# Kernel tuning notes

Measured on AMD Instinct MI355X. Metric: run time of the kernel, lower is better.

The kernel has to match this reference:

```python
import jax, jax.numpy as jnp
import numpy as np

B, N, L, C, H = 2, 3000, 6, 128, 1
IN_DIM = 6
SIGMA_D = 1.0
EPS = 1e-5
DH = C // H


def _conv1(x, W, b):
    # pointwise Conv1d: x [B,Cin,N], W [Cout,Cin], b [Cout]
    return jnp.einsum('oc,bcn->bon', W, x) + b[None, :, None]


def _bn(x, g, beta):
    # BatchNorm1d (training-mode batch stats) over (B, N) per channel
    m = x.mean(axis=(0, 2), keepdims=True)
    v = x.var(axis=(0, 2), keepdims=True)
    return g[None, :, None] * (x - m) * jax.lax.rsqrt(v + EPS) + beta[None, :, None]


def setup_inputs() -> dict:
    key = jax.random.key(0)
    ks = iter(jax.random.split(key, 80))

    def w(shape, fan_in):
        return jax.random.normal(next(ks), shape, jnp.float32) * (1.0 / np.sqrt(fan_in))

    src = jax.random.normal(next(ks), (B, N, 3), jnp.float32)
    tgt = src + 0.1 * jax.random.normal(next(ks), (B, N, 3), jnp.float32)
    corr_pos = jnp.concatenate([src, tgt], axis=-1)  # [B,N,6]

    d = {
        'corr_pos': corr_pos, 'src_keypts': src, 'tgt_keypts': tgt,
        'init_W': w((C, IN_DIM), IN_DIM), 'init_b': jnp.zeros((C,), jnp.float32),
        'pcn_W': w((L, C, C), C), 'pcn_b': jnp.zeros((L, C), jnp.float32),
        'pcn_g': jnp.ones((L, C), jnp.float32), 'pcn_beta': jnp.zeros((L, C), jnp.float32),
        'qW': w((L, C, C), C), 'qb': jnp.zeros((L, C), jnp.float32),
        'kW': w((L, C, C), C), 'kb': jnp.zeros((L, C), jnp.float32),
        'vW': w((L, C, C), C), 'vb': jnp.zeros((L, C), jnp.float32),
        'm1W': w((L, C // 2, C), C), 'm1b': jnp.zeros((L, C // 2), jnp.float32),
        'm1g': jnp.ones((L, C // 2), jnp.float32), 'm1beta': jnp.zeros((L, C // 2), jnp.float32),
        'm2W': w((L, C // 2, C // 2), C // 2), 'm2b': jnp.zeros((L, C // 2), jnp.float32),
        'm2g': jnp.ones((L, C // 2), jnp.float32), 'm2beta': jnp.zeros((L, C // 2), jnp.float32),
        'm3W': w((L, C, C // 2), C // 2), 'm3b': jnp.zeros((L, C), jnp.float32),
        'c1W': w((32, C), C), 'c1b': jnp.zeros((32,), jnp.float32),
        'c2W': w((32, 32), 32), 'c2b': jnp.zeros((32,), jnp.float32),
        'c3W': w((1, 32), 32), 'c3b': jnp.zeros((1,), jnp.float32),
    }
    return d


def reference(corr_pos, src_keypts, tgt_keypts, init_W, init_b,
              pcn_W, pcn_b, pcn_g, pcn_beta,
              qW, qb, kW, kb, vW, vb,
              m1W, m1b, m1g, m1beta, m2W, m2b, m2g, m2beta, m3W, m3b,
              c1W, c1b, c2W, c2b, c3W, c3b):
    # spatial compatibility: clamp(1 - (d_src - d_tgt)^2 / sigma_d^2, min=0)  [B,N,N]
    src_dist = jnp.linalg.norm(src_keypts[:, :, None, :] - src_keypts[:, None, :, :], axis=-1)
    tgt_dist = jnp.linalg.norm(tgt_keypts[:, :, None, :] - tgt_keypts[:, None, :, :], axis=-1)
    sc = jnp.maximum(1.0 - (src_dist - tgt_dist) ** 2 / SIGMA_D ** 2, 0.0)

    # init embedding: [B,C,N]
    x = _conv1(jnp.swapaxes(corr_pos, 1, 2), init_W, init_b)
    scale = 1.0 / jnp.sqrt(jnp.float32(DH))

    for i in range(L):
        # PointCN layer
        x = jax.nn.relu(_bn(_conv1(x, pcn_W[i], pcn_b[i]), pcn_g[i], pcn_beta[i]))
        # NonLocal block
        Q = _conv1(x, qW[i], qb[i]).reshape(B, H, DH, N)
        K = _conv1(x, kW[i], kb[i]).reshape(B, H, DH, N)
        V = _conv1(x, vW[i], vb[i]).reshape(B, H, DH, N)
        scores = jnp.einsum('bhco,bhci->bhoi', Q, K) * scale  # [B,H,N,N]
        weight = jax.nn.softmax(sc[:, None, :, :] * scores, axis=-1)
        msg = jnp.einsum('bhoi,bhci->bhco', weight, V).reshape(B, C, N)
        msg = jax.nn.relu(_bn(_conv1(msg, m1W[i], m1b[i]), m1g[i], m1beta[i]))
        msg = jax.nn.relu(_bn(_conv1(msg, m2W[i], m2b[i]), m2g[i], m2beta[i]))
        msg = _conv1(msg, m3W[i], m3b[i])
        x = x + msg

    corr_feat = x
    norm = jnp.maximum(jnp.linalg.norm(corr_feat, axis=1, keepdims=True), 1e-12)
    normed_corr_feat = corr_feat / norm
    h = jax.nn.relu(_conv1(corr_feat, c1W, c1b))
    h = jax.nn.relu(_conv1(h, c2W, c2b))
    confidence = _conv1(h, c3W, c3b)[:, 0, :]  # [B,N]
    return confidence, normed_corr_feat
```

## Files before the change

kernel.cpp:

```cpp
#include <hip/hip_runtime.h>
#include <hip/hip_bf16.h>


#define BB 2
#define NN 3000
#define CC 128
#define LAYERS 6
#define BN_EPS 1e-5f
#define ATT_SCALE 0.08838834764831845f
#define INV_CNT (1.f / (float)(BB * NN))

typedef _Float16 f16;
typedef _Float16 f16x8 __attribute__((ext_vector_type(8)));
typedef float f32x4 __attribute__((ext_vector_type(4)));

__global__ void init_conv(const float* __restrict__ corr, const float* __restrict__ W,
                          const float* __restrict__ bias, float* __restrict__ x) {
  int idx = blockIdx.x * 256 + threadIdx.x;
  if (idx >= BB * CC * NN) return;
  int n = idx % NN;
  int c = (idx / NN) % CC;
  int b = idx / (NN * CC);
  const float* cp = corr + (b * NN + n) * 6;
  float acc = bias[c];
#pragma unroll
  for (int d = 0; d < 6; ++d) acc += W[c * 6 + d] * cp[d];
  x[idx] = acc;
}

__launch_bounds__(256)
__global__ void conv_mfma_pcn(const float* __restrict__ Xg, float* __restrict__ Y,
                              const float* __restrict__ W, const float* __restrict__ bias,
                              float* __restrict__ osums) {
  __shared__ f16 Xsh[32][136], Xsl[32][136];
  __shared__ f16 Wsh[128][40], Wsl[128][40];
  const int tid = threadIdx.x;
// ... 194 lines not shown
      if (p < BB * NN) {
        int b = p / NN, n = p % NN;
#pragma unroll
        for (int r = 0; r < 4; ++r) {
          int co = co0 + ct * 16 + quad * 4 + r;
          float v = acc[ct][pt][r] + bias[co];
          f16 h = (f16)v;
          f16 lo = (f16)(v - (float)h);
          if (sel == 0) {
            size_t o = (size_t)(b * NN + n) * CC + co;
            Qh[o] = h; Ql[o] = lo;
          } else if (sel == 1) {
            size_t o = (size_t)(b * NN + n) * CC + co;
            Kh[o] = h; Kl[o] = lo;
          } else {
            size_t o = (size_t)(b * CC + co) * NN + n;
            Vh[o] = h; Vl[o] = lo;
          }
        }
      }
    }
}

template <int CIN, int COUT, int NP, int MODE, int CSPLIT, int BNIN, int STATS>
__launch_bounds__(256)
__global__ void conv_k(const float* __restrict__ in, float* __restrict__ out,
                       const float* __restrict__ W, const float* __restrict__ bias,
                       const float* __restrict__ res,
                       const float* __restrict__ isums, const float* __restrict__ ig,
                       const float* __restrict__ ibeta,
                       const float* __restrict__ rsums, const float* __restrict__ rg,
                       const float* __restrict__ rbeta, float* __restrict__ osums) {
  constexpr int COB = COUT / CSPLIT;
  constexpr int CH = (CIN > 64) ? 64 : CIN;
  constexpr int PG = NP / 4;
  constexpr int KPT = COB * PG / 256;
  constexpr int XROW = (NP == 16) ? 20 : 32;
  __shared__ alignas(16) float Xs[CIN][XROW];
  __shared__ float Ws[COB][CH + 1];
  __shared__ float bnsc[BNIN ? CIN : 1], bnsh[BNIN ? CIN : 1];
  const int tid = threadIdx.x;
  const int p0 = blockIdx.x * NP;
  const int co0 = blockIdx.y * COB;

  if (BNIN) {
    for (int c = tid; c < CIN; c += 256) {
      float s = isums[c], s2 = isums[CIN + c];
      float mean = s * INV_CNT;
      float var = s2 * INV_CNT - mean * mean;
      float sc = ig[c] * rsqrtf(var + BN_EPS);
      bnsc[c] = sc;
      bnsh[c] = ibeta[c] - mean * sc;
    }
    __syncthreads();
  }

  for (int idx = tid; idx < CIN * NP; idx += 256) {
    int ci = idx / NP, j = idx % NP;
    int p = p0 + j;
    float v = 0.f;
    if (p < BB * NN) {
      int b = p / NN, n = p % NN;
      v = in[(b * CIN + ci) * NN + n];
      if (BNIN) {
        v = v * bnsc[ci] + bnsh[ci];
        v = v > 0.f ? v : 0.f;
      }
    }
    Xs[ci][j] = v;
  }

  const int nb = (tid % PG) * 4;
  const int cb = (tid / PG) * KPT;

  float acc[KPT][4];
#pragma unroll
  for (int k = 0; k < KPT; ++k)
#pragma unroll
    for (int j = 0; j < 4; ++j) acc[k][j] = 0.f;

  for (int c0 = 0; c0 < CIN; c0 += CH) {
    __syncthreads();
    for (int idx = tid; idx < COB * CH; idx += 256) {
      int co = idx / CH, cc = idx % CH;
      Ws[co][cc] = W[(co0 + co) * CIN + c0 + cc];
    }
    __syncthreads();
#pragma unroll 4
    for (int cc = 0; cc < CH; ++cc) {
      float4 xv = *reinterpret_cast<const float4*>(&Xs[c0 + cc][nb]);
#pragma unroll
      for (int k = 0; k < KPT; ++k) {
        float w = Ws[cb + k][cc];
        acc[k][0] += w * xv.x;
        acc[k][1] += w * xv.y;
        acc[k][2] += w * xv.z;
        acc[k][3] += w * xv.w;
      }
    }
  }

#pragma unroll
  for (int k = 0; k < KPT; ++k) {
    int co = co0 + cb + k;
    float bv = bias[co];
    float rsc = 0.f, rsh = 0.f;
    if (MODE == 3) {
      float s = rsums[co], s2 = rsums[COUT + co];
      float mean = s * INV_CNT;
      float var = s2 * INV_CNT - mean * mean;
      rsc = rg[co] * rsqrtf(var + BN_EPS);
      rsh = rbeta[co] - mean * rsc;
    }
    float sp = 0.f, sp2 = 0.f;
#pragma unroll
    for (int j = 0; j < 4; ++j) {
      int p = p0 + nb + j;
      if (p < BB * NN) {
        int b = p / NN, n = p % NN;
        int o = (b * COUT + co) * NN + n;
        float v = acc[k][j] + bv;
        if (MODE == 3) {
          float rr = res[o] * rsc + rsh;
          v += (rr > 0.f ? rr : 0.f);
        }
        out[o] = v;
        if (STATS) {
          sp += v;
          sp2 += v * v;
        }
      }
    }
    if (STATS) {
#pragma unroll
      for (int d = 1; d < PG; d <<= 1) {
        sp += __shfl_xor(sp, d);
        sp2 += __shfl_xor(sp2, d);
      }
      if ((tid & (PG - 1)) == 0) {
        atomicAdd(&osums[co], sp);
        atomicAdd(&osums[COUT + co], sp2);
      }
    }
  }
}

__launch_bounds__(512)
__global__ void attn_mf7(const f16* __restrict__ Qhp, const f16* __restrict__ Qlp,
                         const f16* __restrict__ Khp, const f16* __restrict__ Klp,
                         const f16* __restrict__ Vhp, const f16* __restrict__ Vlp,
                         const float* __restrict__ srcp, const float* __restrict__ tgtp,
                         float* __restrict__ pacc, float* __restrict__ pm,
                         float* __restrict__ pl, int chunk) {
  const int b = blockIdx.z;
  const int q0 = blockIdx.x * 128;
  const int s = blockIdx.y;
  const int cs = s * chunk;
  const int ce = min(cs + chunk, NN);
  const int tid = threadIdx.x;
  const int w = tid >> 6, lane = tid & 63, quad = lane >> 4, l15 = lane & 15;

  __shared__ f16 Ksh[32][136], Ksl[32][136];
  __shared__ f16 Vsh[128][40], Vsl[128][40];
  __shared__ f16 Ps[8][16][40];
  __shared__ float kps[6][36];

  float qp[4][6];
  const int orow = q0 + w * 16;
#pragma unroll
  for (int r = 0; r < 4; ++r) {
    int o = orow + quad * 4 + r;
    if (o >= NN) o = NN - 1;
#pragma unroll
    for (int d = 0; d < 3; ++d) {
      qp[r][d] = srcp[(b * NN + o) * 3 + d];
      qp[r][3 + d] = tgtp[(b * NN + o) * 3 + d];
    }
  }
  f16x8 qh[4], ql[4];
  {
    int o = orow + l15;
    if (o >= NN) o = NN - 1;
    size_t base = (size_t)(b * NN + o) * CC + quad * 8;
#pragma unroll
    for (int cc = 0; cc < 4; ++cc) {
      qh[cc] = *reinterpret_cast<const f16x8*>(Qhp + base + cc * 32);
      ql[cc] = *reinterpret_cast<const f16x8*>(Qlp + base + cc * 32);
    }
  }

  float m[4], l[4];
#pragma unroll
  for (int r = 0; r < 4; ++r) {
    m[r] = -1e30f;
    l[r] = 0.f;
  }
  f32x4 acco[8];
#pragma unroll
  for (int t = 0; t < 8; ++t) acco[t] = (f32x4){0.f, 0.f, 0.f, 0.f};

  const int NT = (ce - cs + 31) >> 5;
  for (int it = 0; it < NT; ++it) {
    const int kk0 = cs + it * 32;
    __syncthreads();
    for (int t = tid; t < 1024; t += 512) {
      int plane = t >> 9, row = (t >> 4) & 31, cu = t & 15;
      int kr = kk0 + row;
      if (kr >= NN) kr = NN - 1;
      const f16* src = (plane ? Klp : Khp) + (size_t)(b * NN + kr) * CC + cu * 8;
      uint4 v = *reinterpret_cast<const uint4*>(src);
      f16* dst = plane ? &Ksl[row][cu * 8] : &Ksh[row][cu * 8];
      *reinterpret_cast<uint4*>(dst) = v;
    }
    for (int t = tid; t < 1024; t += 512) {
      int plane = t >> 9, c = (t >> 2) & 127, iu = t & 3;
      int kb = kk0 + iu * 8;
      if (kb > NN - 8) kb = NN - 8;
      const f16* src = (plane ? Vlp : Vhp) + (size_t)(b * CC + c) * NN + kb;
      uint4 v = *reinterpret_cast<const uint4*>(src);
      f16* dst = plane ? &Vsl[c][iu * 8] : &Vsh[c][iu * 8];
      *reinterpret_cast<uint4*>(dst) = v;
    }
    if (tid < 192) {
      int d = tid >> 5, i = tid & 31;
      int ig = kk0 + i;
      if (ig >= NN) ig = NN - 1;
      kps[d][i] = (d < 3) ? srcp[(b * NN + ig) * 3 + d] : tgtp[(b * NN + ig) * 3 + d - 3];
    }
    __syncthreads();

    f32x4 accs[2];
#pragma unroll
    for (int k4 = 0; k4 < 2; ++k4) accs[k4] = (f32x4){0.f, 0.f, 0.f, 0.f};
#pragma unroll
    for (int cc = 0; cc < 4; ++cc) {
#pragma unroll
      for (int k4 = 0; k4 < 2; ++k4) {
        f16x8 bh = *reinterpret_cast<const f16x8*>(&Ksh[k4 * 16 + l15][cc * 32 + quad * 8]);
        f16x8 bl = *reinterpret_cast<const f16x8*>(&Ksl[k4 * 16 + l15][cc * 32 + quad * 8]);
        accs[k4] = __builtin_amdgcn_mfma_f32_16x16x32_f16(qh[cc], bl, accs[k4], 0, 0, 0);
        accs[k4] = __builtin_amdgcn_mfma_f32_16x16x32_f16(ql[cc], bh, accs[k4], 0, 0, 0);
        accs[k4] = __builtin_amdgcn_mfma_f32_16x16x32_f16(qh[cc], bh, accs[k4], 0, 0, 0);
      }
    }

    float sv[2][4];
#pragma unroll
    for (int k4 = 0; k4 < 2; ++k4) {
      int iloc = k4 * 16 + l15;
      int ig = kk0 + iloc;
      float kx = kps[0][iloc], ky = kps[1][iloc], kz = kps[2][iloc];
      float tx = kps[3][iloc], ty = kps[4][iloc], tz = kps[5][iloc];
#pragma unroll
      for (int r = 0; r < 4; ++r) {
        float dx = qp[r][0] - kx, dy = qp[r][1] - ky, dz = qp[r][2] - kz;
        float ds2 = dx * dx + dy * dy + dz * dz;
        float ex = qp[r][3] - tx, ey = qp[r][4] - ty, ez = qp[r][5] - tz;
        float dt2 = ex * ex + ey * ey + ez * ez;
        float d2 = ds2 + dt2 - 2.f * sqrtf(ds2 * dt2);
        float gg = 1.f - d2;
        gg = gg > 0.f ? gg : 0.f;
        float val = accs[k4][r] * (ATT_SCALE * gg);
        sv[k4][r] = (ig < ce) ? val : -1e30f;
      }
    }

    float tmax[4];
#pragma unroll
    for (int r = 0; r < 4; ++r) tmax[r] = fmaxf(sv[0][r], sv[1][r]);
#pragma unroll
    for (int d = 1; d <= 8; d <<= 1)
#pragma unroll
      for (int r = 0; r < 4; ++r) tmax[r] = fmaxf(tmax[r], __shfl_xor(tmax[r], d));

    float alpha[4], ps[4];
    f16 pf[2][4];
#pragma unroll
    for (int r = 0; r < 4; ++r) {
      float mn = fmaxf(m[r], tmax[r]);
      alpha[r] = __expf(m[r] - mn);
      m[r] = mn;
      pf[0][r] = (f16)__expf(sv[0][r] - mn);
      pf[1][r] = (f16)__expf(sv[1][r] - mn);
      ps[r] = (float)pf[0][r] + (float)pf[1][r];
    }
#pragma unroll
    for (int d = 1; d <= 8; d <<= 1)
#pragma unroll
      for (int r = 0; r < 4; ++r) ps[r] += __shfl_xor(ps[r], d);
#pragma unroll
    for (int r = 0; r < 4; ++r) {
      l[r] = l[r] * alpha[r] + ps[r];
#pragma unroll
      for (int t = 0; t < 8; ++t) acco[t][r] *= alpha[r];
    }
#pragma unroll
    for (int r = 0; r < 4; ++r) {
      Ps[w][quad * 4 + r][l15] = pf[0][r];
      Ps[w][quad * 4 + r][16 + l15] = pf[1][r];
    }
    __syncthreads();

    {
      f16x8 af = *reinterpret_cast<const f16x8*>(&Ps[w][l15][quad * 8]);
#pragma unroll
      for (int t = 0; t < 8; ++t) {
        f16x8 vh = *reinterpret_cast<const f16x8*>(&Vsh[t * 16 + l15][quad * 8]);
        f16x8 vl = *reinterpret_cast<const f16x8*>(&Vsl[t * 16 + l15][quad * 8]);
        acco[t] = __builtin_amdgcn_mfma_f32_16x16x32_f16(af, vl, acco[t], 0, 0, 0);
        acco[t] = __builtin_amdgcn_mfma_f32_16x16x32_f16(af, vh, acco[t], 0, 0, 0);
      }
    }
  }

  const int pidx = s * BB + b;
  if (l15 == 0) {
#pragma unroll
    for (int r = 0; r < 4; ++r) {
      int o = orow + quad * 4 + r;
      if (o < NN) {
        pm[pidx * NN + o] = m[r];
        pl[pidx * NN + o] = l[r];
      }
    }
  }
#pragma unroll
  for (int r = 0; r < 4; ++r) {
    int o = orow + quad * 4 + r;
    if (o < NN) {
      size_t base2 = ((size_t)pidx * NN + o) * CC;
#pragma unroll
      for (int t = 0; t < 8; ++t) pacc[base2 + t * 16 + l15] = acco[t][r];
    }
  }
}

__launch_bounds__(256)
__global__ void conv_m1(const float* __restrict__ pacc, const float* __restrict__ pm,
                        const float* __restrict__ pl, float* __restrict__ out,
                        const float* __restrict__ W, const float* __restrict__ bias,
                        float* __restrict__ osums, int ksplit) {
  __shared__ alignas(16) float Xs[128][20];
  __shared__ float Ws[64][65];
  __shared__ float Es[16][17];
  __shared__ float Li[16];
  const int tid = threadIdx.x;
  const int p0 = blockIdx.x * 16;

  if (tid < 16) {
    int p = p0 + tid;
    float Lv = 1.f;
    if (p < BB * NN) {
      int b = p / NN, o = p % NN;
      float M = -1e30f;
      for (int s = 0; s < ksplit; ++s) M = fmaxf(M, pm[(s * BB + b) * NN + o]);
      Lv = 0.f;
      for (int s = 0; s < ksplit; ++s) {
        int pi = s * BB + b;
        float e = __expf(pm[pi * NN + o] - M);
        Es[tid][s] = e;
        Lv += pl[pi * NN + o] * e;
      }
    } else {
      for (int s = 0; s < ksplit; ++s) Es[tid][s] = 0.f;
    }
    Li[tid] = 1.f / Lv;
  }
  __syncthreads();

  for (int idx = tid; idx < 512; idx += 256) {
    int j = idx >> 5, c4 = (idx & 31) * 4;
    int p = p0 + j;
    float4 a = {0.f, 0.f, 0.f, 0.f};
    if (p < BB * NN) {
      int b = p / NN, o = p % NN;
      for (int s = 0; s < ksplit; ++s) {
        float e = Es[j][s];
        const float4 pv = *reinterpret_cast<const float4*>(
            &pacc[((size_t)(s * BB + b) * NN + o) * CC + c4]);
        a.x += pv.x * e;
        a.y += pv.y * e;
        a.z += pv.z * e;
        a.w += pv.w * e;
      }
      float inv = Li[j];
      a.x *= inv; a.y *= inv; a.z *= inv; a.w *= inv;
    }
    Xs[c4][j] = a.x;
    Xs[c4 + 1][j] = a.y;
    Xs[c4 + 2][j] = a.z;
    Xs[c4 + 3][j] = a.w;
  }

  const int nb = (tid & 3) * 4;
  const int co = tid >> 2;
  float acc[4] = {0.f, 0.f, 0.f, 0.f};

  for (int c0 = 0; c0 < 128; c0 += 64) {
    __syncthreads();
    for (int idx = tid; idx < 64 * 64; idx += 256) {
      int cr = idx >> 6, cc = idx & 63;
      Ws[cr][cc] = W[cr * 128 + c0 + cc];
    }
    __syncthreads();
#pragma unroll 4
    for (int cc = 0; cc < 64; ++cc) {
      float4 xv = *reinterpret_cast<const float4*>(&Xs[c0 + cc][nb]);
      float w = Ws[co][cc];
      acc[0] += w * xv.x;
      acc[1] += w * xv.y;
      acc[2] += w * xv.z;
      acc[3] += w * xv.w;
    }
  }

  {
    float bv = bias[co];
    float sp = 0.f, sp2 = 0.f;
#pragma unroll
    for (int j = 0; j < 4; ++j) {
      int p = p0 + nb + j;
      if (p < BB * NN) {
        int b = p / NN, n = p % NN;
        float v = acc[j] + bv;
        out[(b * 64 + co) * NN + n] = v;
        sp += v;
        sp2 += v * v;
      }
    }
    sp += __shfl_xor(sp, 1);
    sp2 += __shfl_xor(sp2, 1);
    sp += __shfl_xor(sp, 2);
    sp2 += __shfl_xor(sp2, 2);
    if ((tid & 3) == 0) {
      atomicAdd(&osums[co], sp);
      atomicAdd(&osums[64 + co], sp2);
    }
  }
}

__launch_bounds__(256)
__global__ void head_all(const float* __restrict__ Xg,
                         const float* __restrict__ c1W, const float* __restrict__ c1b,
                         const float* __restrict__ c2W, const float* __restrict__ c2b,
                         const float* __restrict__ c3W, const float* __restrict__ c3b,
                         float* __restrict__ out) {
  __shared__ float Xs[128][33];
  __shared__ float W1[32][129];
  __shared__ float W2[32][33];
  __shared__ float Hs[32][33], H2s[32][33];
  __shared__ float Inv[32];
  const int tid = threadIdx.x;
  const int p0 = blockIdx.x * 32;
  const int j = tid >> 3, sub = tid & 7;

  for (int idx = tid; idx < 128 * 32; idx += 256) {
    int ci = idx >> 5, jj = idx & 31;
    int p = p0 + jj;
    float v = 0.f;
// ... 120 lines not shown
  float* VhF = KlF + PLANE;
  float* VlF = VhF + PLANE;
  float* SB = VlF + PLANE;
  float* pacc = SB + 3072;
  f16* Qh = (f16*)QhF;
  f16* Ql = (f16*)QlF;
  f16* Kh = (f16*)KhF;
  f16* Kl = (f16*)KlF;
  f16* Vh = (f16*)VhF;
  f16* Vl = (f16*)VlF;
  float* T1 = QhF;
  float* T2 = KhF;

  const size_t base_f = (size_t)(2 * FEAT + 6 * PLANE + 3072);
  const size_t per_f = (size_t)BB * NN * CC + 2 * (size_t)BB * NN;
  int ksplit = 16;
  while (ksplit > 1 && (base_f + (size_t)ksplit * per_f) * 4 > ws_size) ksplit >>= 1;
  const int chunk = (((NN + ksplit - 1) / ksplit) + 7) & ~7;
  float* pm = pacc + (size_t)ksplit * BB * NN * CC;
  float* pl = pm + (size_t)ksplit * BB * NN;

  dim3 blk(256);
  const int PT32 = (BB * NN + 31) / 32;
  const int PT16 = (BB * NN + 15) / 16;
  const int G_FEAT = (FEAT + 255) / 256;

  hipMemsetAsync(SB, 0, 3072 * sizeof(float), stream);
  init_conv<<<G_FEAT, blk, 0, stream>>>(corr, initW, initb, X);

  for (int i = 0; i < LAYERS; ++i) {
    float* pcnS = SB + i * 512;
    float* m1S = pcnS + 256;
    float* m2S = m1S + 128;
    conv_mfma_pcn<<<PT32, blk, 0, stream>>>(X, Y, pcnW + i * 16384, pcnb + i * 128, pcnS);
    conv_mfma_qkv<<<dim3(PT32, 3), blk, 0, stream>>>(
        Y, pcnS, pcng + i * 128, pcnbeta + i * 128, qW + i * 16384, kW + i * 16384,
        vW + i * 16384, qb + i * 128, kb + i * 128, vb + i * 128,
        Qh, Ql, Kh, Kl, Vh, Vl);
    attn_mf7<<<dim3((NN + 127) / 128, ksplit, BB), dim3(512), 0, stream>>>(
        Qh, Ql, Kh, Kl, Vh, Vl, srcp, tgtp, pacc, pm, pl, chunk);
    conv_m1<<<PT16, blk, 0, stream>>>(pacc, pm, pl, T1, m1W + i * 8192, m1b + i * 64,
                                      m1S, ksplit);
    conv_k<64, 64, 16, 0, 1, 1, 1><<<dim3(PT16, 1), blk, 0, stream>>>(
        T1, T2, m2W + i * 4096, m2b + i * 64, nullptr,
        m1S, m1g + i * 64, m1beta + i * 64, nullptr, nullptr, nullptr, m2S);
    conv_k<64, 128, 16, 3, 2, 1, 0><<<dim3(PT16, 2), blk, 0, stream>>>(
        T2, X, m3W + i * 8192, m3b + i * 128, Y,
        m2S, m2g + i * 64, m2beta + i * 64, pcnS, pcng + i * 128, pcnbeta + i * 128,
        nullptr);
  }

  head_all<<<PT32, blk, 0, stream>>>(X, c1W, c1b, c2W, c2b, c3W, c3b, (float*)d_out);
}
```

Baseline: 1.296 ms.

## Port message convolutions to split-f16 MFMA and prefetch K/V tiles in attention

Replaces the scalar FP32 conv_m1, conv_k m2 and m3 kernels with MFMA versions that split activations and weights into high and low f16 parts, using three MFMAs to approximate FP32 accuracy. The blocks now cover 32 points instead of 16. The attention kernel gains a register prefetch of the next K/V/position tile, issued before the barrier so global loads overlap with compute. This costs more registers and extra conversion work, and the split-f16 arithmetic may differ slightly numerically from FP32.

```diff
diff --git a/kernel.cpp b/kernel.cpp
--- a/kernel.cpp
+++ b/kernel.cpp
@@ -12,6 +12,7 @@
 
 typedef _Float16 f16;
 typedef _Float16 f16x8 __attribute__((ext_vector_type(8)));
+typedef _Float16 f16x4 __attribute__((ext_vector_type(4)));
 typedef float f32x4 __attribute__((ext_vector_type(4)));
 
 __global__ void init_conv(const float* __restrict__ corr, const float* __restrict__ W,
@@ -252,332 +253,21 @@
     }
 }
 
-template <int CIN, int COUT, int NP, int MODE, int CSPLIT, int BNIN, int STATS>
 __launch_bounds__(256)
-__global__ void conv_k(const float* __restrict__ in, float* __restrict__ out,
-                       const float* __restrict__ W, const float* __restrict__ bias,
-                       const float* __restrict__ res,
-                       const float* __restrict__ isums, const float* __restrict__ ig,
-                       const float* __restrict__ ibeta,
-                       const float* __restrict__ rsums, const float* __restrict__ rg,
-                       const float* __restrict__ rbeta, float* __restrict__ osums) {
-  constexpr int COB = COUT / CSPLIT;
-  constexpr int CH = (CIN > 64) ? 64 : CIN;
-  constexpr int PG = NP / 4;
-  constexpr int KPT = COB * PG / 256;
-  constexpr int XROW = (NP == 16) ? 20 : 32;
-  __shared__ alignas(16) float Xs[CIN][XROW];
-  __shared__ float Ws[COB][CH + 1];
-  __shared__ float bnsc[BNIN ? CIN : 1], bnsh[BNIN ? CIN : 1];
+__global__ void conv_mfma_m1(const float* __restrict__ pacc, const float* __restrict__ pm,
+                             const float* __restrict__ pl, float* __restrict__ out,
+                             const float* __restrict__ W, const float* __restrict__ bias,
+                             float* __restrict__ osums, int ksplit) {
+  __shared__ f16 Xsh[32][136], Xsl[32][136];
+  __shared__ f16 Wsh[64][40], Wsl[64][40];
+  __shared__ float Es[32][17];
+  __shared__ float Li[32];
   const int tid = threadIdx.x;
-  const int p0 = blockIdx.x * NP;
-  const int co0 = blockIdx.y * COB;
-
-  if (BNIN) {
-    for (int c = tid; c < CIN; c += 256) {
-      float s = isums[c], s2 = isums[CIN + c];
-      float mean = s * INV_CNT;
-      float var = s2 * INV_CNT - mean * mean;
-      float sc = ig[c] * rsqrtf(var + BN_EPS);
-      bnsc[c] = sc;
-      bnsh[c] = ibeta[c] - mean * sc;
-    }
-    __syncthreads();
-  }
-
-  for (int idx = tid; idx < CIN * NP; idx += 256) {
-    int ci = idx / NP, j = idx % NP;
-    int p = p0 + j;
-    float v = 0.f;
-    if (p < BB * NN) {
-      int b = p / NN, n = p % NN;
-      v = in[(b * CIN + ci) * NN + n];
-      if (BNIN) {
-        v = v * bnsc[ci] + bnsh[ci];
-        v = v > 0.f ? v : 0.f;
-      }
-    }
-    Xs[ci][j] = v;
-  }
-
-  const int nb = (tid % PG) * 4;
-  const int cb = (tid / PG) * KPT;
-
-  float acc[KPT][4];
-#pragma unroll
-  for (int k = 0; k < KPT; ++k)
-#pragma unroll
-    for (int j = 0; j < 4; ++j) acc[k][j] = 0.f;
-
-  for (int c0 = 0; c0 < CIN; c0 += CH) {
-    __syncthreads();
-    for (int idx = tid; idx < COB * CH; idx += 256) {
-      int co = idx / CH, cc = idx % CH;
-      Ws[co][cc] = W[(co0 + co) * CIN + c0 + cc];
-    }
-    __syncthreads();
-#pragma unroll 4
-    for (int cc = 0; cc < CH; ++cc) {
-      float4 xv = *reinterpret_cast<const float4*>(&Xs[c0 + cc][nb]);
-#pragma unroll
-      for (int k = 0; k < KPT; ++k) {
-        float w = Ws[cb + k][cc];
-        acc[k][0] += w * xv.x;
-        acc[k][1] += w * xv.y;
-        acc[k][2] += w * xv.z;
-        acc[k][3] += w * xv.w;
-      }
-    }
-  }
-
-#pragma unroll
-  for (int k = 0; k < KPT; ++k) {
-    int co = co0 + cb + k;
-    float bv = bias[co];
-    float rsc = 0.f, rsh = 0.f;
-    if (MODE == 3) {
-      float s = rsums[co], s2 = rsums[COUT + co];
-      float mean = s * INV_CNT;
-      float var = s2 * INV_CNT - mean * mean;
-      rsc = rg[co] * rsqrtf(var + BN_EPS);
-      rsh = rbeta[co] - mean * rsc;
-    }
-    float sp = 0.f, sp2 = 0.f;
-#pragma unroll
-    for (int j = 0; j < 4; ++j) {
-      int p = p0 + nb + j;
-      if (p < BB * NN) {
-        int b = p / NN, n = p % NN;
-        int o = (b * COUT + co) * NN + n;
-        float v = acc[k][j] + bv;
-        if (MODE == 3) {
-          float rr = res[o] * rsc + rsh;
-          v += (rr > 0.f ? rr : 0.f);
-        }
-        out[o] = v;
-        if (STATS) {
-          sp += v;
-          sp2 += v * v;
-        }
-      }
-    }
-    if (STATS) {
-#pragma unroll
-      for (int d = 1; d < PG; d <<= 1) {
-        sp += __shfl_xor(sp, d);
-        sp2 += __shfl_xor(sp2, d);
-      }
-      if ((tid & (PG - 1)) == 0) {
-        atomicAdd(&osums[co], sp);
-        atomicAdd(&osums[COUT + co], sp2);
-      }
-    }
-  }
-}
-
-__launch_bounds__(512)
-__global__ void attn_mf7(const f16* __restrict__ Qhp, const f16* __restrict__ Qlp,
-                         const f16* __restrict__ Khp, const f16* __restrict__ Klp,
-                         const f16* __restrict__ Vhp, const f16* __restrict__ Vlp,
-                         const float* __restrict__ srcp, const float* __restrict__ tgtp,
-                         float* __restrict__ pacc, float* __restrict__ pm,
-                         float* __restrict__ pl, int chunk) {
-  const int b = blockIdx.z;
-  const int q0 = blockIdx.x * 128;
-  const int s = blockIdx.y;
-  const int cs = s * chunk;
-  const int ce = min(cs + chunk, NN);
-  const int tid = threadIdx.x;
+  const int p0 = blockIdx.x * 32;
   const int w = tid >> 6, lane = tid & 63, quad = lane >> 4, l15 = lane & 15;
-
-  __shared__ f16 Ksh[32][136], Ksl[32][136];
-  __shared__ f16 Vsh[128][40], Vsl[128][40];
-  __shared__ f16 Ps[8][16][40];
-  __shared__ float kps[6][36];
-
-  float qp[4][6];
-  const int orow = q0 + w * 16;
-#pragma unroll
-  for (int r = 0; r < 4; ++r) {
-    int o = orow + quad * 4 + r;
-    if (o >= NN) o = NN - 1;
-#pragma unroll
-    for (int d = 0; d < 3; ++d) {
-      qp[r][d] = srcp[(b * NN + o) * 3 + d];
-      qp[r][3 + d] = tgtp[(b * NN + o) * 3 + d];
-    }
-  }
-  f16x8 qh[4], ql[4];
-  {
-    int o = orow + l15;
-    if (o >= NN) o = NN - 1;
-    size_t base = (size_t)(b * NN + o) * CC + quad * 8;
-#pragma unroll
-    for (int cc = 0; cc < 4; ++cc) {
-      qh[cc] = *reinterpret_cast<const f16x8*>(Qhp + base + cc * 32);
-      ql[cc] = *reinterpret_cast<const f16x8*>(Qlp + base + cc * 32);
-    }
-  }
-
-  float m[4], l[4];
-#pragma unroll
-  for (int r = 0; r < 4; ++r) {
-    m[r] = -1e30f;
-    l[r] = 0.f;
-  }
-  f32x4 acco[8];
-#pragma unroll
-  for (int t = 0; t < 8; ++t) acco[t] = (f32x4){0.f, 0.f, 0.f, 0.f};
-
-  const int NT = (ce - cs + 31) >> 5;
-  for (int it = 0; it < NT; ++it) {
-    const int kk0 = cs + it * 32;
-    __syncthreads();
-    for (int t = tid; t < 1024; t += 512) {
-      int plane = t >> 9, row = (t >> 4) & 31, cu = t & 15;
-      int kr = kk0 + row;
-      if (kr >= NN) kr = NN - 1;
-      const f16* src = (plane ? Klp : Khp) + (size_t)(b * NN + kr) * CC + cu * 8;
-      uint4 v = *reinterpret_cast<const uint4*>(src);
-      f16* dst = plane ? &Ksl[row][cu * 8] : &Ksh[row][cu * 8];
-      *reinterpret_cast<uint4*>(dst) = v;
-    }
-    for (int t = tid; t < 1024; t += 512) {
-      int plane = t >> 9, c = (t >> 2) & 127, iu = t & 3;
-      int kb = kk0 + iu * 8;
-      if (kb > NN - 8) kb = NN - 8;
-      const f16* src = (plane ? Vlp : Vhp) + (size_t)(b * CC + c) * NN + kb;
-      uint4 v = *reinterpret_cast<const uint4*>(src);
-      f16* dst = plane ? &Vsl[c][iu * 8] : &Vsh[c][iu * 8];
-      *reinterpret_cast<uint4*>(dst) = v;
-    }
-    if (tid < 192) {
-      int d = tid >> 5, i = tid & 31;
-      int ig = kk0 + i;
-      if (ig >= NN) ig = NN - 1;
-      kps[d][i] = (d < 3) ? srcp[(b * NN + ig) * 3 + d] : tgtp[(b * NN + ig) * 3 + d - 3];
-    }
-    __syncthreads();
-
-    f32x4 accs[2];
-#pragma unroll
-    for (int k4 = 0; k4 < 2; ++k4) accs[k4] = (f32x4){0.f, 0.f, 0.f, 0.f};
-#pragma unroll
-    for (int cc = 0; cc < 4; ++cc) {
-#pragma unroll
-      for (int k4 = 0; k4 < 2; ++k4) {
-        f16x8 bh = *reinterpret_cast<const f16x8*>(&Ksh[k4 * 16 + l15][cc * 32 + quad * 8]);
-        f16x8 bl = *reinterpret_cast<const f16x8*>(&Ksl[k4 * 16 + l15][cc * 32 + quad * 8]);
-        accs[k4] = __builtin_amdgcn_mfma_f32_16x16x32_f16(qh[cc], bl, accs[k4], 0, 0, 0);
-        accs[k4] = __builtin_amdgcn_mfma_f32_16x16x32_f16(ql[cc], bh, accs[k4], 0, 0, 0);
-        accs[k4] = __builtin_amdgcn_mfma_f32_16x16x32_f16(qh[cc], bh, accs[k4], 0, 0, 0);
-      }
-    }
-
-    float sv[2][4];
-#pragma unroll
-    for (int k4 = 0; k4 < 2; ++k4) {
-      int iloc = k4 * 16 + l15;
-      int ig = kk0 + iloc;
-      float kx = kps[0][iloc], ky = kps[1][iloc], kz = kps[2][iloc];
-      float tx = kps[3][iloc], ty = kps[4][iloc], tz = kps[5][iloc];
-#pragma unroll
-      for (int r = 0; r < 4; ++r) {
-        float dx = qp[r][0] - kx, dy = qp[r][1] - ky, dz = qp[r][2] - kz;
-        float ds2 = dx * dx + dy * dy + dz * dz;
-        float ex = qp[r][3] - tx, ey = qp[r][4] - ty, ez = qp[r][5] - tz;
-        float dt2 = ex * ex + ey * ey + ez * ez;
-        float d2 = ds2 + dt2 - 2.f * sqrtf(ds2 * dt2);
-        float gg = 1.f - d2;
-        gg = gg > 0.f ? gg : 0.f;
-        float val = accs[k4][r] * (ATT_SCALE * gg);
-        sv[k4][r] = (ig < ce) ? val : -1e30f;
-      }
-    }
-
-    float tmax[4];
-#pragma unroll
-    for (int r = 0; r < 4; ++r) tmax[r] = fmaxf(sv[0][r], sv[1][r]);
-#pragma unroll
-    for (int d = 1; d <= 8; d <<= 1)
-#pragma unroll
-      for (int r = 0; r < 4; ++r) tmax[r] = fmaxf(tmax[r], __shfl_xor(tmax[r], d));
-
-    float alpha[4], ps[4];
-    f16 pf[2][4];
-#pragma unroll
-    for (int r = 0; r < 4; ++r) {
-      float mn = fmaxf(m[r], tmax[r]);
-      alpha[r] = __expf(m[r] - mn);
-      m[r] = mn;
-      pf[0][r] = (f16)__expf(sv[0][r] - mn);
-      pf[1][r] = (f16)__expf(sv[1][r] - mn);
-      ps[r] = (float)pf[0][r] + (float)pf[1][r];
-    }
-#pragma unroll
-    for (int d = 1; d <= 8; d <<= 1)
-#pragma unroll
-      for (int r = 0; r < 4; ++r) ps[r] += __shfl_xor(ps[r], d);
-#pragma unroll
-    for (int r = 0; r < 4; ++r) {
-      l[r] = l[r] * alpha[r] + ps[r];
-#pragma unroll
-      for (int t = 0; t < 8; ++t) acco[t][r] *= alpha[r];
-    }
-#pragma unroll
-    for (int r = 0; r < 4; ++r) {
-      Ps[w][quad * 4 + r][l15] = pf[0][r];
-      Ps[w][quad * 4 + r][16 + l15] = pf[1][r];
-    }
-    __syncthreads();
-
-    {
-      f16x8 af = *reinterpret_cast<const f16x8*>(&Ps[w][l15][quad * 8]);
-#pragma unroll
-      for (int t = 0; t < 8; ++t) {
-        f16x8 vh = *reinterpret_cast<const f16x8*>(&Vsh[t * 16 + l15][quad * 8]);
-        f16x8 vl = *reinterpret_cast<const f16x8*>(&Vsl[t * 16 + l15][quad * 8]);
-        acco[t] = __builtin_amdgcn_mfma_f32_16x16x32_f16(af, vl, acco[t], 0, 0, 0);
-        acco[t] = __builtin_amdgcn_mfma_f32_16x16x32_f16(af, vh, acco[t], 0, 0, 0);
-      }
-    }
-  }
-
-  const int pidx = s * BB + b;
-  if (l15 == 0) {
-#pragma unroll
-    for (int r = 0; r < 4; ++r) {
-      int o = orow + quad * 4 + r;
-      if (o < NN) {
-        pm[pidx * NN + o] = m[r];
-        pl[pidx * NN + o] = l[r];
-      }
-    }
-  }
-#pragma unroll
-  for (int r = 0; r < 4; ++r) {
-    int o = orow + quad * 4 + r;
-    if (o < NN) {
-      size_t base2 = ((size_t)pidx * NN + o) * CC;
-#pragma unroll
-      for (int t = 0; t < 8; ++t) pacc[base2 + t * 16 + l15] = acco[t][r];
-    }
-  }
-}
-
-__launch_bounds__(256)
-__global__ void conv_m1(const float* __restrict__ pacc, const float* __restrict__ pm,
-                        const float* __restrict__ pl, float* __restrict__ out,
-                        const float* __restrict__ W, const float* __restrict__ bias,
-                        float* __restrict__ osums, int ksplit) {
-  __shared__ alignas(16) float Xs[128][20];
-  __shared__ float Ws[64][65];
-  __shared__ float Es[16][17];
-  __shared__ float Li[16];
-  const int tid = threadIdx.x;
-  const int p0 = blockIdx.x * 16;
-
-  if (tid < 16) {
+  const int co0 = w * 16;
+
+  if (tid < 32) {
     int p = p0 + tid;
     float Lv = 1.f;
     if (p < BB * NN) {
@@ -598,7 +288,7 @@
   }
   __syncthreads();
 
-  for (int idx = tid; idx < 512; idx += 256) {
+  for (int idx = tid; idx < 1024; idx += 256) {
     int j = idx >> 5, c4 = (idx & 31) * 4;
     int p = p0 + j;
     float4 a = {0.f, 0.f, 0.f, 0.f};
@@ -616,55 +306,516 @@
       float inv = Li[j];
       a.x *= inv; a.y *= inv; a.z *= inv; a.w *= inv;
     }
-    Xs[c4][j] = a.x;
-    Xs[c4 + 1][j] = a.y;
-    Xs[c4 + 2][j] = a.z;
-    Xs[c4 + 3][j] = a.w;
-  }
-
-  const int nb = (tid & 3) * 4;
-  const int co = tid >> 2;
-  float acc[4] = {0.f, 0.f, 0.f, 0.f};
-
-  for (int c0 = 0; c0 < 128; c0 += 64) {
-    __syncthreads();
-    for (int idx = tid; idx < 64 * 64; idx += 256) {
-      int cr = idx >> 6, cc = idx & 63;
-      Ws[cr][cc] = W[cr * 128 + c0 + cc];
-    }
-    __syncthreads();
-#pragma unroll 4
-    for (int cc = 0; cc < 64; ++cc) {
-      float4 xv = *reinterpret_cast<const float4*>(&Xs[c0 + cc][nb]);
-      float w = Ws[co][cc];
-      acc[0] += w * xv.x;
-      acc[1] += w * xv.y;
-      acc[2] += w * xv.z;
-      acc[3] += w * xv.w;
-    }
-  }
-
+    float av[4] = {a.x, a.y, a.z, a.w};
+    f16x4 hv, lv;
+#pragma unroll
+    for (int t = 0; t < 4; ++t) {
+      f16 h = (f16)av[t];
+      hv[t] = h;
+      lv[t] = (f16)(av[t] - (float)h);
+    }
+    *reinterpret_cast<f16x4*>(&Xsh[j][c4]) = hv;
+    *reinterpret_cast<f16x4*>(&Xsl[j][c4]) = lv;
+  }
+
+  f32x4 acc[2];
+#pragma unroll
+  for (int pt = 0; pt < 2; ++pt) acc[pt] = (f32x4){0.f, 0.f, 0.f, 0.f};
+
+  for (int kc = 0; kc < 4; ++kc) {
+    __syncthreads();
+    for (int idx = tid; idx < 256; idx += 256) {
+      int co = idx >> 2, ks = idx & 3;
+      const float* wp = W + co * 128 + kc * 32 + ks * 8;
+      float4 w0 = *reinterpret_cast<const float4*>(wp);
+      float4 w1 = *reinterpret_cast<const float4*>(wp + 4);
+      float wv[8] = {w0.x, w0.y, w0.z, w0.w, w1.x, w1.y, w1.z, w1.w};
+      f16x8 hv, lv;
+#pragma unroll
+      for (int t = 0; t < 8; ++t) {
+        f16 h = (f16)wv[t];
+        hv[t] = h;
+        lv[t] = (f16)(wv[t] - (float)h);
+      }
+      *reinterpret_cast<f16x8*>(&Wsh[co][ks * 8]) = hv;
+      *reinterpret_cast<f16x8*>(&Wsl[co][ks * 8]) = lv;
+    }
+    __syncthreads();
+    f16x8 ah = *reinterpret_cast<const f16x8*>(&Wsh[co0 + l15][quad * 8]);
+    f16x8 al = *reinterpret_cast<const f16x8*>(&Wsl[co0 + l15][quad * 8]);
+#pragma unroll
+    for (int pt = 0; pt < 2; ++pt) {
+      f16x8 bh = *reinterpret_cast<const f16x8*>(&Xsh[pt * 16 + l15][kc * 32 + quad * 8]);
+      f16x8 bl = *reinterpret_cast<const f16x8*>(&Xsl[pt * 16 + l15][kc * 32 + quad * 8]);
+      acc[pt] = __builtin_amdgcn_mfma_f32_16x16x32_f16(ah, bl, acc[pt], 0, 0, 0);
+      acc[pt] = __builtin_amdgcn_mfma_f32_16x16x32_f16(al, bh, acc[pt], 0, 0, 0);
+      acc[pt] = __builtin_amdgcn_mfma_f32_16x16x32_f16(ah, bh, acc[pt], 0, 0, 0);
+    }
+  }
+
+  float sp[4] = {0.f, 0.f, 0.f, 0.f}, sp2[4] = {0.f, 0.f, 0.f, 0.f};
+#pragma unroll
+  for (int pt = 0; pt < 2; ++pt) {
+    int p = p0 + pt * 16 + l15;
+    if (p < BB * NN) {
+      int b = p / NN, n = p % NN;
+#pragma unroll
+      for (int r = 0; r < 4; ++r) {
+        int co = co0 + quad * 4 + r;
+        float v = acc[pt][r] + bias[co];
+        out[(b * 64 + co) * NN + n] = v;
+        sp[r] += v;
+        sp2[r] += v * v;
+      }
+    }
+  }
+#pragma unroll
+  for (int r = 0; r < 4; ++r)
+#pragma unroll
+    for (int d = 1; d <= 8; d <<= 1) {
+      sp[r] += __shfl_xor(sp[r], d);
+      sp2[r] += __shfl_xor(sp2[r], d);
+    }
+  if (l15 == 0) {
+#pragma unroll
+    for (int r = 0; r < 4; ++r) {
+      int co = co0 + quad * 4 + r;
+      atomicAdd(&osums[co], sp[r]);
+      atomicAdd(&osums[64 + co], sp2[r]);
+    }
+  }
+}
+
+__launch_bounds__(256)
+__global__ void conv_mfma_m2(const float* __restrict__ Tin, const float* __restrict__ isums,
+                             const float* __restrict__ ig, const float* __restrict__ ibeta,
+                             float* __restrict__ out, const float* __restrict__ W,
+                             const float* __restrict__ bias, float* __restrict__ osums) {
+  __shared__ f16 Xsh[32][72], Xsl[32][72];
+  __shared__ f16 Wsh[64][40], Wsl[64][40];
+  __shared__ float bnsc[64], bnsh[64];
+  const int tid = threadIdx.x;
+  const int p0 = blockIdx.x * 32;
+  const int w = tid >> 6, lane = tid & 63, quad = lane >> 4, l15 = lane & 15;
+  const int co0 = w * 16;
+
+  if (tid < 64) {
+    float s = isums[tid], s2 = isums[64 + tid];
+    float mean = s * INV_CNT;
+    float var = s2 * INV_CNT - mean * mean;
+    float sc = ig[tid] * rsqrtf(var + BN_EPS);
+    bnsc[tid] = sc;
+    bnsh[tid] = ibeta[tid] - mean * sc;
+  }
+  __syncthreads();
+
+  for (int idx = tid; idx < 256; idx += 256) {
+    int ci = (idx >> 5) * 8, j = idx & 31;
+    int p = p0 + j;
+    if (p >= BB * NN) p = BB * NN - 1;
+    int b = p / NN, n = p % NN;
+    f16x8 hv, lv;
+#pragma unroll
+    for (int t = 0; t < 8; ++t) {
+      float v = Tin[(b * 64 + ci + t) * NN + n];
+      v = v * bnsc[ci + t] + bnsh[ci + t];
+      v = v > 0.f ? v : 0.f;
+      f16 h = (f16)v;
+      hv[t] = h;
+      lv[t] = (f16)(v - (float)h);
+    }
+    *reinterpret_cast<f16x8*>(&Xsh[j][ci]) = hv;
+    *reinterpret_cast<f16x8*>(&Xsl[j][ci]) = lv;
+  }
+
+  f32x4 acc[2];
+#pragma unroll
+  for (int pt = 0; pt < 2; ++pt) acc[pt] = (f32x4){0.f, 0.f, 0.f, 0.f};
+
+  for (int kc = 0; kc < 2; ++kc) {
+    __syncthreads();
+    for (int idx = tid; idx < 256; idx += 256) {
+      int co = idx >> 2, ks = idx & 3;
+      const float* wp = W + co * 64 + kc * 32 + ks * 8;
+      float4 w0 = *reinterpret_cast<const float4*>(wp);
+      float4 w1 = *reinterpret_cast<const float4*>(wp + 4);
+      float wv[8] = {w0.x, w0.y, w0.z, w0.w, w1.x, w1.y, w1.z, w1.w};
+      f16x8 hv, lv;
+#pragma unroll
+      for (int t = 0; t < 8; ++t) {
+        f16 h = (f16)wv[t];
+        hv[t] = h;
+        lv[t] = (f16)(wv[t] - (float)h);
+      }
+      *reinterpret_cast<f16x8*>(&Wsh[co][ks * 8]) = hv;
+      *reinterpret_cast<f16x8*>(&Wsl[co][ks * 8]) = lv;
+    }
+    __syncthreads();
+    f16x8 ah = *reinterpret_cast<const f16x8*>(&Wsh[co0 + l15][quad * 8]);
+    f16x8 al = *reinterpret_cast<const f16x8*>(&Wsl[co0 + l15][quad * 8]);
+#pragma unroll
+    for (int pt = 0; pt < 2; ++pt) {
+      f16x8 bh = *reinterpret_cast<const f16x8*>(&Xsh[pt * 16 + l15][kc * 32 + quad * 8]);
+      f16x8 bl = *reinterpret_cast<const f16x8*>(&Xsl[pt * 16 + l15][kc * 32 + quad * 8]);
+      acc[pt] = __builtin_amdgcn_mfma_f32_16x16x32_f16(ah, bl, acc[pt], 0, 0, 0);
+      acc[pt] = __builtin_amdgcn_mfma_f32_16x16x32_f16(al, bh, acc[pt], 0, 0, 0);
+      acc[pt] = __builtin_amdgcn_mfma_f32_16x16x32_f16(ah, bh, acc[pt], 0, 0, 0);
+    }
+  }
+
+  float sp[4] = {0.f, 0.f, 0.f, 0.f}, sp2[4] = {0.f, 0.f, 0.f, 0.f};
+#pragma unroll
+  for (int pt = 0; pt < 2; ++pt) {
+    int p = p0 + pt * 16 + l15;
+    if (p < BB * NN) {
+      int b = p / NN, n = p % NN;
+#pragma unroll
+      for (int r = 0; r < 4; ++r) {
+        int co = co0 + quad * 4 + r;
+        float v = acc[pt][r] + bias[co];
+        out[(b * 64 + co) * NN + n] = v;
+        sp[r] += v;
+        sp2[r] += v * v;
+      }
+    }
+  }
+#pragma unroll
+  for (int r = 0; r < 4; ++r)
+#pragma unroll
+    for (int d = 1; d <= 8; d <<= 1) {
+      sp[r] += __shfl_xor(sp[r], d);
+      sp2[r] += __shfl_xor(sp2[r], d);
+    }
+  if (l15 == 0) {
+#pragma unroll
+    for (int r = 0; r < 4; ++r) {
+      int co = co0 + quad * 4 + r;
+      atomicAdd(&osums[co], sp[r]);
+      atomicAdd(&osums[64 + co], sp2[r]);
+    }
+  }
+}
+
+__launch_bounds__(256)
+__global__ void conv_mfma_m3(const float* __restrict__ Tin, const float* __restrict__ isums,
+                             const float* __restrict__ ig, const float* __restrict__ ibeta,
+                             const float* __restrict__ Yres, const float* __restrict__ rsums,
+                             const float* __restrict__ rg, const float* __restrict__ rbeta,
+                             float* __restrict__ out, const float* __restrict__ W,
+                             const float* __restrict__ bias) {
+  __shared__ f16 Xsh[32][72], Xsl[32][72];
+  __shared__ f16 Wsh[128][40], Wsl[128][40];
+  __shared__ float bnsc[64], bnsh[64];
+  const int tid = threadIdx.x;
+  const int p0 = blockIdx.x * 32;
+  const int w = tid >> 6, lane = tid & 63, quad = lane >> 4, l15 = lane & 15;
+  const int co0 = w * 32;
+
+  if (tid < 64) {
+    float s = isums[tid], s2 = isums[64 + tid];
+    float mean = s * INV_CNT;
+    float var = s2 * INV_CNT - mean * mean;
+    float sc = ig[tid] * rsqrtf(var + BN_EPS);
+    bnsc[tid] = sc;
+    bnsh[tid] = ibeta[tid] - mean * sc;
+  }
+  __syncthreads();
+
+  for (int idx = tid; idx < 256; idx += 256) {
+    int ci = (idx >> 5) * 8, j = idx & 31;
+    int p = p0 + j;
+    if (p >= BB * NN) p = BB * NN - 1;
+    int b = p / NN, n = p % NN;
+    f16x8 hv, lv;
+#pragma unroll
+    for (int t = 0; t < 8; ++t) {
+      float v = Tin[(b * 64 + ci + t) * NN + n];
+      v = v * bnsc[ci + t] + bnsh[ci + t];
+      v = v > 0.f ? v : 0.f;
+      f16 h = (f16)v;
+      hv[t] = h;
+      lv[t] = (f16)(v - (float)h);
+    }
+    *reinterpret_cast<f16x8*>(&Xsh[j][ci]) = hv;
+    *reinterpret_cast<f16x8*>(&Xsl[j][ci]) = lv;
+  }
+
+  f32x4 acc[2][2];
+#pragma unroll
+  for (int ct = 0; ct < 2; ++ct)
+#pragma unroll
+    for (int pt = 0; pt < 2; ++pt) acc[ct][pt] = (f32x4){0.f, 0.f, 0.f, 0.f};
+
+  for (int kc = 0; kc < 2; ++kc) {
+    __syncthreads();
+    for (int idx = tid; idx < 512; idx += 256) {
+      int co = idx >> 2, ks = idx & 3;
+      const float* wp = W + co * 64 + kc * 32 + ks * 8;
+      float4 w0 = *reinterpret_cast<const float4*>(wp);
+      float4 w1 = *reinterpret_cast<const float4*>(wp + 4);
+      float wv[8] = {w0.x, w0.y, w0.z, w0.w, w1.x, w1.y, w1.z, w1.w};
+      f16x8 hv, lv;
+#pragma unroll
+      for (int t = 0; t < 8; ++t) {
+        f16 h = (f16)wv[t];
+        hv[t] = h;
+        lv[t] = (f16)(wv[t] - (float)h);
+      }
+      *reinterpret_cast<f16x8*>(&Wsh[co][ks * 8]) = hv;
+      *reinterpret_cast<f16x8*>(&Wsl[co][ks * 8]) = lv;
+    }
+    __syncthreads();
+#pragma unroll
+    for (int ct = 0; ct < 2; ++ct) {
+      f16x8 ah = *reinterpret_cast<const f16x8*>(&Wsh[co0 + ct * 16 + l15][quad * 8]);
+      f16x8 al = *reinterpret_cast<const f16x8*>(&Wsl[co0 + ct * 16 + l15][quad * 8]);
+#pragma unroll
+      for (int pt = 0; pt < 2; ++pt) {
+        f16x8 bh = *reinterpret_cast<const f16x8*>(&Xsh[pt * 16 + l15][kc * 32 + quad * 8]);
+        f16x8 bl = *reinterpret_cast<const f16x8*>(&Xsl[pt * 16 + l15][kc * 32 + quad * 8]);
+        acc[ct][pt] = __builtin_amdgcn_mfma_f32_16x16x32_f16(ah, bl, acc[ct][pt], 0, 0, 0);
+        acc[ct][pt] = __builtin_amdgcn_mfma_f32_16x16x32_f16(al, bh, acc[ct][pt], 0, 0, 0);
+        acc[ct][pt] = __builtin_amdgcn_mfma_f32_16x16x32_f16(ah, bh, acc[ct][pt], 0, 0, 0);
+      }
+    }
+  }
+
+#pragma unroll
+  for (int ct = 0; ct < 2; ++ct) {
+#pragma unroll
+    for (int r = 0; r < 4; ++r) {
+      int co = co0 + ct * 16 + quad * 4 + r;
+      float s = rsums[co], s2 = rsums[128 + co];
+      float mean = s * INV_CNT;
+      float var = s2 * INV_CNT - mean * mean;
+      float rsc = rg[co] * rsqrtf(var + BN_EPS);
+      float rsh = rbeta[co] - mean * rsc;
+      float bv = bias[co];
+#pragma unroll
+      for (int pt = 0; pt < 2; ++pt) {
+        int p = p0 + pt * 16 + l15;
+        if (p < BB * NN) {
+          int b = p / NN, n = p % NN;
+          int o = (b * 128 + co) * NN + n;
+          float rr = Yres[o] * rsc + rsh;
+          out[o] = acc[ct][pt][r] + bv + (rr > 0.f ? rr : 0.f);
+        }
+      }
+    }
+  }
+}
+
+__launch_bounds__(512)
+__global__ void attn_mf8(const f16* __restrict__ Qhp, const f16* __restrict__ Qlp,
+                         const f16* __restrict__ Khp, const f16* __restrict__ Klp,
+                         const f16* __restrict__ Vhp, const f16* __restrict__ Vlp,
+                         const float* __restrict__ srcp, const float* __restrict__ tgtp,
+                         float* __restrict__ pacc, float* __restrict__ pm,
+                         float* __restrict__ pl, int chunk) {
+  const int b = blockIdx.z;
+  const int q0 = blockIdx.x * 128;
+  const int s = blockIdx.y;
+  const int cs = s * chunk;
+  const int ce = min(cs + chunk, NN);
+  const int tid = threadIdx.x;
+  const int w = tid >> 6, lane = tid & 63, quad = lane >> 4, l15 = lane & 15;
+
+  __shared__ f16 Ksh[32][136], Ksl[32][136];
+  __shared__ f16 Vsh[128][40], Vsl[128][40];
+  __shared__ f16 Ps[8][16][40];
+  __shared__ float kps[6][36];
+
+  float qp[4][6];
+  const int orow = q0 + w * 16;
+#pragma unroll
+  for (int r = 0; r < 4; ++r) {
+    int o = orow + quad * 4 + r;
+    if (o >= NN) o = NN - 1;
+#pragma unroll
+    for (int d = 0; d < 3; ++d) {
+      qp[r][d] = srcp[(b * NN + o) * 3 + d];
+      qp[r][3 + d] = tgtp[(b * NN + o) * 3 + d];
+    }
+  }
+  f16x8 qh[4], ql[4];
   {
-    float bv = bias[co];
-    float sp = 0.f, sp2 = 0.f;
-#pragma unroll
-    for (int j = 0; j < 4; ++j) {
-      int p = p0 + nb + j;
-      if (p < BB * NN) {
-        int b = p / NN, n = p % NN;
-        float v = acc[j] + bv;
-        out[(b * 64 + co) * NN + n] = v;
-        sp += v;
-        sp2 += v * v;
-      }
-    }
-    sp += __shfl_xor(sp, 1);
-    sp2 += __shfl_xor(sp2, 1);
-    sp += __shfl_xor(sp, 2);
-    sp2 += __shfl_xor(sp2, 2);
-    if ((tid & 3) == 0) {
-      atomicAdd(&osums[co], sp);
-      atomicAdd(&osums[64 + co], sp2);
+    int o = orow + l15;
+    if (o >= NN) o = NN - 1;
+    size_t base = (size_t)(b * NN + o) * CC + quad * 8;
+#pragma unroll
+    for (int cc = 0; cc < 4; ++cc) {
+      qh[cc] = *reinterpret_cast<const f16x8*>(Qhp + base + cc * 32);
+      ql[cc] = *reinterpret_cast<const f16x8*>(Qlp + base + cc * 32);
+    }
+  }
+
+  float m[4], l[4];
+#pragma unroll
+  for (int r = 0; r < 4; ++r) {
+    m[r] = -1e30f;
+    l[r] = 0.f;
+  }
+  f32x4 acco[8];
+#pragma unroll
+  for (int t = 0; t < 8; ++t) acco[t] = (f32x4){0.f, 0.f, 0.f, 0.f};
+
+  uint4 pk[2], pv[2];
+  float pp = 0.f;
+  auto issue = [&](int kk0) {
+#pragma unroll
+    for (int i2 = 0; i2 < 2; ++i2) {
+      int t = tid + i2 * 512;
+      int plane = t >> 9, row = (t >> 4) & 31, cu = t & 15;
+      int kr = kk0 + row;
+      if (kr >= NN) kr = NN - 1;
+      const f16* src = (plane ? Klp : Khp) + (size_t)(b * NN + kr) * CC + cu * 8;
+      pk[i2] = *reinterpret_cast<const uint4*>(src);
+    }
+#pragma unroll
+    for (int i2 = 0; i2 < 2; ++i2) {
+      int t = tid + i2 * 512;
+      int plane = t >> 9, c = (t >> 2) & 127, iu = t & 3;
+      int kb = kk0 + iu * 8;
+      if (kb > NN - 8) kb = NN - 8;
+      const f16* src = (plane ? Vlp : Vhp) + (size_t)(b * CC + c) * NN + kb;
+      pv[i2] = *reinterpret_cast<const uint4*>(src);
+    }
+    if (tid < 192) {
+      int d = tid >> 5, i = tid & 31;
+      int ig = kk0 + i;
+      if (ig >= NN) ig = NN - 1;
+      pp = (d < 3) ? srcp[(b * NN + ig) * 3 + d] : tgtp[(b * NN + ig) * 3 + d - 3];
+    }
+  };
+
+  const int NT = (ce - cs + 31) >> 5;
+  issue(cs);
+  for (int it = 0; it < NT; ++it) {
+    const int kk0 = cs + it * 32;
+    __syncthreads();
+#pragma unroll
+    for (int i2 = 0; i2 < 2; ++i2) {
+      int t = tid + i2 * 512;
+      int plane = t >> 9, row = (t >> 4) & 31, cu = t & 15;
+      f16* dst = plane ? &Ksl[row][cu * 8] : &Ksh[row][cu * 8];
+      *reinterpret_cast<uint4*>(dst) = pk[i2];
+    }
+#pragma unroll
+    for (int i2 = 0; i2 < 2; ++i2) {
+      int t = tid + i2 * 512;
+      int plane = t >> 9, c = (t >> 2) & 127, iu = t & 3;
+      f16* dst = plane ? &Vsl[c][iu * 8] : &Vsh[c][iu * 8];
+      *reinterpret_cast<uint4*>(dst) = pv[i2];
+    }
+    if (tid < 192) {
+      int d = tid >> 5, i = tid & 31;
+      kps[d][i] = pp;
+    }
+    if (it + 1 < NT) issue(kk0 + 32);
+    __syncthreads();
+
+    f32x4 accs[2];
+#pragma unroll
+    for (int k4 = 0; k4 < 2; ++k4) accs[k4] = (f32x4){0.f, 0.f, 0.f, 0.f};
+#pragma unroll
+    for (int cc = 0; cc < 4; ++cc) {
+#pragma unroll
+      for (int k4 = 0; k4 < 2; ++k4) {
+        f16x8 bh = *reinterpret_cast<const f16x8*>(&Ksh[k4 * 16 + l15][cc * 32 + quad * 8]);
+        f16x8 bl = *reinterpret_cast<const f16x8*>(&Ksl[k4 * 16 + l15][cc * 32 + quad * 8]);
+        accs[k4] = __builtin_amdgcn_mfma_f32_16x16x32_f16(qh[cc], bl, accs[k4], 0, 0, 0);
+        accs[k4] = __builtin_amdgcn_mfma_f32_16x16x32_f16(ql[cc], bh, accs[k4], 0, 0, 0);
+        accs[k4] = __builtin_amdgcn_mfma_f32_16x16x32_f16(qh[cc], bh, accs[k4], 0, 0, 0);
+      }
+    }
+
+    float sv[2][4];
+#pragma unroll
+    for (int k4 = 0; k4 < 2; ++k4) {
+      int iloc = k4 * 16 + l15;
+      int ig = kk0 + iloc;
+      float kx = kps[0][iloc], ky = kps[1][iloc], kz = kps[2][iloc];
+      float tx = kps[3][iloc], ty = kps[4][iloc], tz = kps[5][iloc];
+#pragma unroll
+      for (int r = 0; r < 4; ++r) {
+        float dx = qp[r][0] - kx, dy = qp[r][1] - ky, dz = qp[r][2] - kz;
+        float ds2 = dx * dx + dy * dy + dz * dz;
+        float ex = qp[r][3] - tx, ey = qp[r][4] - ty, ez = qp[r][5] - tz;
+        float dt2 = ex * ex + ey * ey + ez * ez;
+        float d2 = ds2 + dt2 - 2.f * sqrtf(ds2 * dt2);
+        float gg = 1.f - d2;
+        gg = gg > 0.f ? gg : 0.f;
+        float val = accs[k4][r] * (ATT_SCALE * gg);
+        sv[k4][r] = (ig < ce) ? val : -1e30f;
+      }
+    }
+
+    float tmax[4];
+#pragma unroll
+    for (int r = 0; r < 4; ++r) tmax[r] = fmaxf(sv[0][r], sv[1][r]);
+#pragma unroll
+    for (int d = 1; d <= 8; d <<= 1)
+#pragma unroll
+      for (int r = 0; r < 4; ++r) tmax[r] = fmaxf(tmax[r], __shfl_xor(tmax[r], d));
+
+    float alpha[4], ps[4];
+    f16 pf[2][4];
+#pragma unroll
+    for (int r = 0; r < 4; ++r) {
+      float mn = fmaxf(m[r], tmax[r]);
+      alpha[r] = __expf(m[r] - mn);
+      m[r] = mn;
+      pf[0][r] = (f16)__expf(sv[0][r] - mn);
+      pf[1][r] = (f16)__expf(sv[1][r] - mn);
+      ps[r] = (float)pf[0][r] + (float)pf[1][r];
+    }
+#pragma unroll
+    for (int d = 1; d <= 8; d <<= 1)
+#pragma unroll
+      for (int r = 0; r < 4; ++r) ps[r] += __shfl_xor(ps[r], d);
+#pragma unroll
+    for (int r = 0; r < 4; ++r) {
+      l[r] = l[r] * alpha[r] + ps[r];
+#pragma unroll
+      for (int t = 0; t < 8; ++t) acco[t][r] *= alpha[r];
+    }
+#pragma unroll
+    for (int r = 0; r < 4; ++r) {
+      Ps[w][quad * 4 + r][l15] = pf[0][r];
+      Ps[w][quad * 4 + r][16 + l15] = pf[1][r];
+    }
+    __syncthreads();
+
+    {
+      f16x8 af = *reinterpret_cast<const f16x8*>(&Ps[w][l15][quad * 8]);
+#pragma unroll
+      for (int t = 0; t < 8; ++t) {
+        f16x8 vh = *reinterpret_cast<const f16x8*>(&Vsh[t * 16 + l15][quad * 8]);
+        f16x8 vl = *reinterpret_cast<const f16x8*>(&Vsl[t * 16 + l15][quad * 8]);
+        acco[t] = __builtin_amdgcn_mfma_f32_16x16x32_f16(af, vl, acco[t], 0, 0, 0);
+        acco[t] = __builtin_amdgcn_mfma_f32_16x16x32_f16(af, vh, acco[t], 0, 0, 0);
+      }
+    }
+  }
+
+  const int pidx = s * BB + b;
+  if (l15 == 0) {
+#pragma unroll
+    for (int r = 0; r < 4; ++r) {
+      int o = orow + quad * 4 + r;
+      if (o < NN) {
+        pm[pidx * NN + o] = m[r];
+        pl[pidx * NN + o] = l[r];
+      }
+    }
+  }
+#pragma unroll
+  for (int r = 0; r < 4; ++r) {
+    int o = orow + quad * 4 + r;
+    if (o < NN) {
+      size_t base2 = ((size_t)pidx * NN + o) * CC;
+#pragma unroll
+      for (int t = 0; t < 8; ++t) pacc[base2 + t * 16 + l15] = acco[t][r];
     }
   }
 }
@@ -831,7 +982,6 @@
 
   dim3 blk(256);
   const int PT32 = (BB * NN + 31) / 32;
-  const int PT16 = (BB * NN + 15) / 16;
   const int G_FEAT = (FEAT + 255) / 256;
 
   hipMemsetAsync(SB, 0, 3072 * sizeof(float), stream);
@@ -846,17 +996,15 @@
         Y, pcnS, pcng + i * 128, pcnbeta + i * 128, qW + i * 16384, kW + i * 16384,
         vW + i * 16384, qb + i * 128, kb + i * 128, vb + i * 128,
         Qh, Ql, Kh, Kl, Vh, Vl);
-    attn_mf7<<<dim3((NN + 127) / 128, ksplit, BB), dim3(512), 0, stream>>>(
+    attn_mf8<<<dim3((NN + 127) / 128, ksplit, BB), dim3(512), 0, stream>>>(
         Qh, Ql, Kh, Kl, Vh, Vl, srcp, tgtp, pacc, pm, pl, chunk);
-    conv_m1<<<PT16, blk, 0, stream>>>(pacc, pm, pl, T1, m1W + i * 8192, m1b + i * 64,
-                                      m1S, ksplit);
-    conv_k<64, 64, 16, 0, 1, 1, 1><<<dim3(PT16, 1), blk, 0, stream>>>(
-        T1, T2, m2W + i * 4096, m2b + i * 64, nullptr,
-        m1S, m1g + i * 64, m1beta + i * 64, nullptr, nullptr, nullptr, m2S);
-    conv_k<64, 128, 16, 3, 2, 1, 0><<<dim3(PT16, 2), blk, 0, stream>>>(
-        T2, X, m3W + i * 8192, m3b + i * 128, Y,
-        m2S, m2g + i * 64, m2beta + i * 64, pcnS, pcng + i * 128, pcnbeta + i * 128,
-        nullptr);
+    conv_mfma_m1<<<PT32, blk, 0, stream>>>(pacc, pm, pl, T1, m1W + i * 8192,
+                                           m1b + i * 64, m1S, ksplit);
+    conv_mfma_m2<<<PT32, blk, 0, stream>>>(T1, m1S, m1g + i * 64, m1beta + i * 64,
+                                           T2, m2W + i * 4096, m2b + i * 64, m2S);
+    conv_mfma_m3<<<PT32, blk, 0, stream>>>(T2, m2S, m2g + i * 64, m2beta + i * 64,
+                                           Y, pcnS, pcng + i * 128, pcnbeta + i * 128,
+                                           X, m3W + i * 8192, m3b + i * 128);
   }
 
   head_all<<<PT32, blk, 0, stream>>>(X, c1W, c1b, c2W, c2b, c3W, c3b, (float*)d_out);
```

Result: slower. 1.448 ms (+11.7%).
